# Optimization experiments

Hardware: AMD Instinct MI355X
Metric: run time of the kernel (lower is better)

Reference implementation:

```python
import jax, jax.numpy as jnp
import numpy as np


def setup_inputs() -> dict:
    key = jax.random.key(0)
    k1, k2, k3 = jax.random.split(key, 3)
    N, F, E, G = 4096, 128, 131072, 4
    x = jax.random.normal(k1, (N, F), dtype=jnp.float32)
    edge_index = jax.random.randint(k2, (2, E), 0, N, dtype=jnp.int32)
    batch = jnp.sort(jax.random.randint(k3, (N,), 0, G, dtype=jnp.int32))
    return {"x": x, "edge_index": edge_index, "batch": batch}


def reference(x, edge_index, batch):
    # Original torch module: builds a dense [G, N, N] adjacency with
    # max_num_nodes = total N, then torch.where(adj==0, 1, adj) makes every
    # per-graph slice all-ones, so each graph g contributes ALL N*N pairs
    # (row-major order, matching torch.where on a dense matrix), concatenated
    # over graphs. updated_edge_weights is never assigned -> always None, so we
    # return just the rewired edge index.
    N = x.shape[0]
    G = int(jnp.max(batch)) + 1  # num_graphs (data-dependent output size)
    idx = jnp.arange(N, dtype=edge_index.dtype)
    rows = jnp.repeat(idx, N)          # [N*N] : 0,0,...,0,1,1,...
    cols = jnp.tile(idx, N)            # [N*N] : 0,1,...,N-1,0,1,...
    pairs = jnp.stack([rows, cols])    # [2, N*N]
    rewired_edge_index = jnp.tile(pairs, (1, G))  # [2, G*N*N]
    return rewired_edge_index
```

## Files before the change

kernel.cpp:

```cpp
#include <hip/hip_runtime.h>


typedef int v4i __attribute__((ext_vector_type(4)));

__device__ __forceinline__ v4i fa_val(unsigned j, unsigned half,
                                      int shiftN, int maskN) {
    if (j < half) {
        int r = (int)((j >> shiftN) & (unsigned)maskN);
        return (v4i){r, r, r, r};
    } else {
        int c = (int)((j - half) & (unsigned)maskN);
        return (v4i){c, c + 1, c + 2, c + 3};
    }
}

__global__ __launch_bounds__(256) void fa_pow2_kernel(
    int* __restrict__ out,
    unsigned n4,
    unsigned half,
    int shiftN,
    int maskN)
{
    unsigned tid = blockIdx.x * blockDim.x + threadIdx.x;
    unsigned T   = gridDim.x * blockDim.x;
    unsigned g   = tid;
    for (; g + 3u * T < n4; g += 4u * T) {
        #pragma unroll
        for (unsigned u = 0; u < 4; ++u) {
            unsigned j = (g + u * T) << 2;
            *(v4i*)(out + j) = fa_val(j, half, shiftN, maskN);
        }
    }
    for (; g < n4; g += T) {
        unsigned j = g << 2;
        *(v4i*)(out + j) = fa_val(j, half, shiftN, maskN);
    }
}

__global__ __launch_bounds__(256) void fa_generic_kernel(
    int* __restrict__ out, long long n, long long half, long long N)
{
    long long tid    = (long long)blockIdx.x * blockDim.x + threadIdx.x;
    long long stride = (long long)gridDim.x * blockDim.x;
    long long NN = N * N;
    for (long long j = tid; j < n; j += stride) {
        int val;
        if (j < half) val = (int)((j % NN) / N);
        else          val = (int)((j - half) % N);
        out[j] = val;
    }
}

extern "C" void kernel_launch(void* const* d_in, const int* in_sizes, int n_in,
                              void* d_out, int out_size, void* d_ws, size_t ws_size,
                              hipStream_t stream) {
    (void)d_in; (void)d_ws; (void)ws_size;
    int* out = (int*)d_out;
    long long n = (long long)out_size;
    long long half = n / 2;
    long long N = (n_in >= 3) ? (long long)in_sizes[2] : 4096;

    bool pow2 = (N > 0) && ((N & (N - 1)) == 0);
    bool aligned = (n % 4 == 0) && (half % 4 == 0) && (N % 4 == 0);

    if (pow2 && aligned) {
        int shiftN = 0;
        while ((1LL << shiftN) < N) ++shiftN;
        int maskN = (int)(N - 1);
        long long n4 = n >> 2;
        int block = 256;
        long long grid = (n4 + block - 1) / block;
        if (grid > 2048) grid = 2048;
        fa_pow2_kernel<<<(dim3)(unsigned)grid, block, 0, stream>>>(
            out, (unsigned)n4, (unsigned)half, shiftN, maskN);
    } else {
        int block = 256;
        long long grid = (n + block - 1) / block;
        if (grid > 2048) grid = 2048;
        fa_generic_kernel<<<(dim3)(unsigned)grid, block, 0, stream>>>(
            out, n, half, N);
    }
}
```

Measured before the change: 532.4 us.

## Assign contiguous output chunks per block with uniform row/column branch

Replaces the grid-stride 2048-block fill kernel with a 256-block kernel where each block writes one contiguous chunk of the output. A block-uniform branch selects the row half or the column half, so the per-element half check goes away. The goal is more sequential DRAM write streams and less per-store index arithmetic. With only 256 blocks of 256 threads, the risk is too little occupancy to saturate write bandwidth on a large-CU GPU.

```diff
diff --git a/kernel.cpp b/kernel.cpp
--- a/kernel.cpp
+++ b/kernel.cpp
@@ -3,37 +3,37 @@
 
 typedef int v4i __attribute__((ext_vector_type(4)));
 
-__device__ __forceinline__ v4i fa_val(unsigned j, unsigned half,
-                                      int shiftN, int maskN) {
-    if (j < half) {
-        int r = (int)((j >> shiftN) & (unsigned)maskN);
-        return (v4i){r, r, r, r};
-    } else {
-        int c = (int)((j - half) & (unsigned)maskN);
-        return (v4i){c, c + 1, c + 2, c + 3};
-    }
-}
-
-__global__ __launch_bounds__(256) void fa_pow2_kernel(
+__global__ __launch_bounds__(256) void fa_chunk_kernel(
     int* __restrict__ out,
-    unsigned n4,
+    unsigned chunk,
     unsigned half,
     int shiftN,
     int maskN)
 {
-    unsigned tid = blockIdx.x * blockDim.x + threadIdx.x;
-    unsigned T   = gridDim.x * blockDim.x;
-    unsigned g   = tid;
-    for (; g + 3u * T < n4; g += 4u * T) {
-        #pragma unroll
-        for (unsigned u = 0; u < 4; ++u) {
-            unsigned j = (g + u * T) << 2;
-            *(v4i*)(out + j) = fa_val(j, half, shiftN, maskN);
+    unsigned base = blockIdx.x * chunk;
+    unsigned end  = base + chunk;
+    unsigned wave = threadIdx.x >> 6;
+    unsigned lane = threadIdx.x & 63u;
+    unsigned e = base + wave * 256u + lane * 4u;
+
+    if (base < half) {
+        for (; e < end; e += 4096u) {
+            #pragma unroll
+            for (unsigned u = 0; u < 4; ++u) {
+                unsigned j = e + u * 1024u;
+                int r = (int)((j >> shiftN) & (unsigned)maskN);
+                *(v4i*)(out + j) = (v4i){r, r, r, r};
+            }
         }
-    }
-    for (; g < n4; g += T) {
-        unsigned j = g << 2;
-        *(v4i*)(out + j) = fa_val(j, half, shiftN, maskN);
+    } else {
+        for (; e < end; e += 4096u) {
+            #pragma unroll
+            for (unsigned u = 0; u < 4; ++u) {
+                unsigned j = e + u * 1024u;
+                int c = (int)((j - half) & (unsigned)maskN);
+                *(v4i*)(out + j) = (v4i){c, c + 1, c + 2, c + 3};
+            }
+        }
     }
 }
 
@@ -60,19 +60,17 @@
     long long half = n / 2;
     long long N = (n_in >= 3) ? (long long)in_sizes[2] : 4096;
 
-    bool pow2 = (N > 0) && ((N & (N - 1)) == 0);
-    bool aligned = (n % 4 == 0) && (half % 4 == 0) && (N % 4 == 0);
+    const long long GRID = 256;
+    bool pow2 = (N >= 256) && ((N & (N - 1)) == 0);
+    bool divisible = (n % (GRID * 4096) == 0);
 
-    if (pow2 && aligned) {
+    if (pow2 && divisible) {
+        long long chunk = n / GRID;
         int shiftN = 0;
         while ((1LL << shiftN) < N) ++shiftN;
         int maskN = (int)(N - 1);
-        long long n4 = n >> 2;
-        int block = 256;
-        long long grid = (n4 + block - 1) / block;
-        if (grid > 2048) grid = 2048;
-        fa_pow2_kernel<<<(dim3)(unsigned)grid, block, 0, stream>>>(
-            out, (unsigned)n4, (unsigned)half, shiftN, maskN);
+        fa_chunk_kernel<<<(dim3)(unsigned)GRID, 256, 0, stream>>>(
+            out, (unsigned)chunk, (unsigned)half, shiftN, maskN);
     } else {
         int block = 256;
         long long grid = (n + block - 1) / block;
```

New measurement: 514.8 us. -3.3%, faster.
